# Optimization experiments

Measured on AMD Instinct MI355X. Metric: run time of the kernel, lower is better.

## Reference

```python
import jax, jax.numpy as jnp
import numpy as np

EPS = 1e-9
LN_EPS = 1e-5

def _ln(t, g, b):
    m = t.mean(-1, keepdims=True)
    v = ((t - m) ** 2).mean(-1, keepdims=True)
    return (t - m) / jnp.sqrt(v + LN_EPS) * g + b

def _dwconv(t, w, b):
    # t: (B,S,H), w: (H,1,4) depthwise. torch pads 3 on both sides then slices [:S],
    # which equals causal left-pad of 3.
    y = jax.lax.conv_general_dilated(
        t.transpose(0, 2, 1), w, window_strides=(1,), padding=[(3, 0)],
        feature_group_count=w.shape[0], dimension_numbers=("NCH", "OIH", "NCH"))
    return y.transpose(0, 2, 1) + b

def _forward(x, Wq, Wk, Wv, Wo, Wg, We1, We2, Wd1, Wd2, Wa1, Wa2,
             conv_w, conv_b, qn_g, qn_b, kn_g, kn_b, mW1, mb1, mW2, mb2, chunk_size):
    B, S, D = x.shape
    H = Wk.shape[1]
    M = mW1.shape[0]
    q = x @ Wq; k = x @ Wk; v = x @ Wv
    eta = jax.nn.softplus((x @ We1) @ We2)
    delta = jax.nn.softplus((x @ Wd1) @ Wd2)
    alpha = jax.nn.sigmoid((x @ Wa1) @ Wa2)
    q = _ln(_dwconv(q, conv_w, conv_b), qn_g, qn_b)  # computed but unused downstream, as in source
    k = _ln(_dwconv(k, conv_w, conv_b), kn_g, kn_b)
    v = _dwconv(v, conv_w, conv_b)
    n = S // chunk_size
    chunk = lambda t: t.reshape(B, n, chunk_size, H).transpose(1, 0, 2, 3)  # (n,B,C,H)
    xs = (chunk(k), chunk(v), chunk(eta), chunk(delta), chunk(alpha))
    state0 = (jnp.broadcast_to(mW1, (B, M, H)), jnp.broadcast_to(mb1, (B, M)),
              jnp.broadcast_to(mW2, (B, H, M)), jnp.broadcast_to(mb2, (B, H)))

    def step(state, inp):
        W1, b1, W2, b2 = state
        kc, vc, ec, dc, ac = inp  # each (B,C,H)
        inter = jnp.einsum("bch,bmh->bcm", kc, W1) + b1[:, None, :]
        act = jax.nn.gelu(inter, approximate=False)
        out = jnp.einsum("bcm,bhm->bch", act, W2) + b2[:, None, :]
        err = out - vc
        en = jnp.sqrt(jnp.sum(err * err, axis=-1, keepdims=True))  # (B,C,1)
        grad = jnp.where(en > dc, dc * err / (en + EPS), err)
        aw = ac[:, -1, :].mean(-1)[:, None, None]
        ew = ec[:, -1, :].mean(-1)[:, None, None]
        us = grad.mean(1, keepdims=True)   # (B,1,H)
        am = act.mean(1, keepdims=True)    # (B,1,M)
        W1g = jnp.einsum("bom,boh->bmh", am, us)
        W2g = jnp.einsum("boh,bom->bhm", us, am)
        nW1 = aw * W1 - ew * W1g
        nW2 = aw * W2 - ew * W2g
        ab = ac[:, -1, :]; eb = ec[:, -1, :]
        b2u = grad.mean(1)
        b1u = jnp.einsum("bch,bhm->bcm", grad, nW2).mean(1)
        nb2 = ab * b2 - eb * b2u
        nb1 = ab.mean(-1, keepdims=True) * b1 - eb.mean(-1, keepdims=True) * b1u
        # torch updates state under no_grad -> detach
        new_state = jax.tree_util.tree_map(jax.lax.stop_gradient, (nW1, nb1, nW2, nb2))
        return new_state, out

    _, outs = jax.lax.scan(step, state0, xs)  # (n,B,C,H)
    combined = outs.transpose(1, 0, 2, 3).reshape(B, S, H)
    return (combined @ Wo) * jax.nn.sigmoid(x @ Wg)

def setup_inputs():
    key = jax.random.key(0)
    B, S, D, H, M, R = 4, 4096, 1024, 128, 256, 64
    ks = jax.random.split(key, 23)
    g = lambda i, shp, s: jax.random.normal(ks[i], shp, jnp.float32) * s
    return {
        "x": g(0, (B, S, D), 1.0),
        "Wq": g(1, (D, H), 0.02), "Wk": g(2, (D, H), 0.02), "Wv": g(3, (D, H), 0.02),
        "Wo": g(4, (H, D), 0.02), "Wg": g(5, (D, D), 0.02),
        "We1": g(6, (D, R), 0.02), "We2": g(7, (R, H), 0.02),
        "Wd1": g(8, (D, R), 0.02), "Wd2": g(9, (R, H), 0.02),
        "Wa1": g(10, (D, R), 0.02), "Wa2": g(11, (R, H), 0.02),
        "conv_w": g(12, (H, 1, 4), 0.2), "conv_b": g(13, (H,), 0.02),
        "qn_g": jnp.ones((H,), jnp.float32), "qn_b": jnp.zeros((H,), jnp.float32),
        "kn_g": jnp.ones((H,), jnp.float32), "kn_b": jnp.zeros((H,), jnp.float32),
        "mW1": g(14, (M, H), 0.05), "mb1": g(15, (M,), 0.02),
        "mW2": g(16, (H, M), 0.05), "mb2": g(17, (H,), 0.02),
        "chunk_size": 64,
    }

def reference(x, Wq, Wk, Wv, Wo, Wg, We1, We2, Wd1, Wd2, Wa1, Wa2,
              conv_w, conv_b, qn_g, qn_b, kn_g, kn_b, mW1, mb1, mW2, mb2, chunk_size):
    return _forward(x, Wq, Wk, Wv, Wo, Wg, We1, We2, Wd1, Wd2, Wa1, Wa2,
                    conv_w, conv_b, qn_g, qn_b, kn_g, kn_b, mW1, mb1, mW2, mb2, chunk_size)
```

## Files before the change

kernel.cpp:

```cpp
#include <hip/hip_runtime.h>
#include <math.h>

#define Bq 4
#define Sq 4096
#define Dq 1024
#define Hq 128
#define Mq 256
#define Rq 64
#define Cq 64
#define NCHUNK 64
#define BSq (Bq*Sq)

typedef __attribute__((ext_vector_type(8))) short short8;
typedef __attribute__((ext_vector_type(4))) float f32x4;
typedef __attribute__((ext_vector_type(2))) unsigned int uintx2;

#define U_WKVTH  ((size_t)0)
#define U_WKVTL  (U_WKVTH + (size_t)2*Hq*Dq)
#define U_WEDATH (U_WKVTL + (size_t)2*Hq*Dq)
#define U_WEDATL (U_WEDATH + (size_t)3*Rq*Dq)
#define U_WGTH   (U_WEDATL + (size_t)3*Rq*Dq)
#define U_WGTL   (U_WGTH + (size_t)Dq*Dq)
#define U_WE2TH  (U_WGTL + (size_t)Dq*Dq)
#define U_WE2TL  (U_WE2TH + (size_t)Hq*Rq)
#define U_WD2TH  (U_WE2TL + (size_t)Hq*Rq)
#define U_WD2TL  (U_WD2TH + (size_t)Hq*Rq)
#define U_WA2TH  (U_WD2TL + (size_t)Hq*Rq)
#define U_WA2TL  (U_WA2TH + (size_t)Hq*Rq)
#define U_WOTH   (U_WA2TL + (size_t)Hq*Rq)
#define U_WOTL   (U_WOTH + (size_t)Dq*Hq)
#define U_END    (U_WOTL + (size_t)Dq*Hq)

__device__ __forceinline__ float softplusf_(float x){
  return fmaxf(x,0.f) + log1pf(expf(-fabsf(x)));
}
__device__ __forceinline__ float sigmoidf_(float x){
  return 1.f/(1.f+__expf(-x));
}
__device__ __forceinline__ unsigned short bf16rn(float x){
  unsigned u = __float_as_uint(x);
  u += 0x7fffu + ((u>>16)&1u);
  return (unsigned short)(u>>16);
}
__device__ __forceinline__ float bf16tof(unsigned short s){
  return __uint_as_float(((unsigned)s)<<16);
}
__device__ __forceinline__ unsigned cvt_pk_bf16(float a, float b){
  unsigned r;
  asm("v_cvt_pk_bf16_f32 %0, %1, %2" : "=v"(r) : "v"(a), "v"(b));
  return r;
}
__device__ __forceinline__ float lo16f(unsigned p){ return __uint_as_float(p<<16); }
__device__ __forceinline__ float hi16f(unsigned p){ return __uint_as_float(p & 0xffff0000u); }
union pk8 { unsigned u[4]; short8 s; };

__device__ __forceinline__ float gelu_fast(float x){
  float z  = x*0.70710678118f;
  float az = fabsf(z);
  float t  = __builtin_amdgcn_rcpf(fmaf(0.3275911f, az, 1.f));
  float p  = fmaf(t, 1.061405429f, -1.453152027f);
  p = fmaf(t, p, 1.421413741f);
  p = fmaf(t, p, -0.284496736f);
  p = fmaf(t, p, 0.254829592f);
  p = p*t;
  float e  = __expf(-az*az);
  float er = copysignf(1.f - p*e, z);
  return 0.5f*x*(1.f + er);
}

template<int BN, int ACT>
__global__ __launch_bounds__(256) void gemm_bf3(
    const float* __restrict__ Af,
    const unsigned short* __restrict__ BhT, const unsigned short* __restrict__ BlT,
    float* __restrict__ C, const float* __restrict__ gate, int N, int K)
{
  constexpr int BM = 128;
  constexpr int PK = 40;
  constexpr int TN = BN/32;
  __shared__ __align__(16) unsigned short As[2][BM*PK];
  __shared__ __align__(16) unsigned short Bs[2][BN*PK];
  const int tid = threadIdx.x;
  const int bm = blockIdx.y*BM, bn = blockIdx.x*BN;
  const int wv = tid>>6, lane = tid&63;
  const int n16 = lane&15, q = lane>>4;
  const int wm = wv>>1, wn = wv&1;

  f32x4 acc[4][TN];
  #pragma unroll
  for (int i=0;i<4;i++){
    #pragma unroll
    for (int j=0;j<TN;j++){ f32x4 z={0.f,0.f,0.f,0.f}; acc[i][j]=z; }
  }
  for (int k0=0;k0<K;k0+=32){
    #pragma unroll
    for (int c0=0;c0<BM*8;c0+=256){
      int c = c0 + tid;
      int row = c>>3, kg = (c&7)*4;
      float4 v = *(const float4*)&Af[(size_t)(bm+row)*K + k0+kg];
      unsigned hp0 = cvt_pk_bf16(v.x, v.y), hp1 = cvt_pk_bf16(v.z, v.w);
      unsigned lp0 = cvt_pk_bf16(v.x-lo16f(hp0), v.y-hi16f(hp0));
      unsigned lp1 = cvt_pk_bf16(v.z-lo16f(hp1), v.w-hi16f(hp1));
      int off = row*PK+kg;
      uintx2 th = {hp0, hp1}, tl = {lp0, lp1};
      *(uintx2*)&As[0][off] = th;
      *(uintx2*)&As[1][off] = tl;
    }
    #pragma unroll
    for (int c0=0;c0<BN*4;c0+=256){
      int c = c0 + tid;
      int row = c>>2, kg = (c&3)*8;
      *(short8*)&Bs[0][row*PK+kg] = *(const short8*)&BhT[(size_t)(bn+row)*K + k0+kg];
      *(short8*)&Bs[1][row*PK+kg] = *(const short8*)&BlT[(size_t)(bn+row)*K + k0+kg];
    }
    __syncthreads();
    short8 a_h[4], a_l[4], b_h[TN], b_l[TN];
    #pragma unroll
    for (int i=0;i<4;i++){
      int r = wm*64 + i*16 + n16;
      a_h[i] = *(const short8*)&As[0][r*PK + q*8];
      a_l[i] = *(const short8*)&As[1][r*PK + q*8];
    }
    #pragma unroll
    for (int j=0;j<TN;j++){
      int r = wn*(BN/2) + j*16 + n16;
      b_h[j] = *(const short8*)&Bs[0][r*PK + q*8];
      b_l[j] = *(const short8*)&Bs[1][r*PK + q*8];
    }
    #pragma unroll
    for (int i=0;i<4;i++){
      #pragma unroll
      for (int j=0;j<TN;j++){
        acc[i][j] = __builtin_amdgcn_mfma_f32_16x16x32_bf16(a_h[i], b_h[j], acc[i][j], 0,0,0);
        acc[i][j] = __builtin_amdgcn_mfma_f32_16x16x32_bf16(a_l[i], b_h[j], acc[i][j], 0,0,0);
        acc[i][j] = __builtin_amdgcn_mfma_f32_16x16x32_bf16(a_h[i], b_l[j], acc[i][j], 0,0,0);
      }
    }
    __syncthreads();
  }
  #pragma unroll
  for (int i=0;i<4;i++){
    #pragma unroll
    for (int j=0;j<TN;j++){
      #pragma unroll
      for (int r=0;r<4;r++){
        int row = bm + wm*64 + i*16 + q*4 + r;
        int col = bn + wn*(BN/2) + j*16 + n16;
        float v = acc[i][j][r];
        if (ACT==1) v = softplusf_(v);
        else if (ACT==2) v = sigmoidf_(v);
        else if (ACT==3) v *= sigmoidf_(gate[(size_t)row*N+col]);
        C[(size_t)row*N+col] = v;
      }
    }
  }
}

template<int BN>
__global__ __launch_bounds__(256) void gemm_bb(
    const unsigned short* __restrict__ Ah, const unsigned short* __restrict__ Al,
    const unsigned short* __restrict__ BhT, const unsigned short* __restrict__ BlT,
    float* __restrict__ C0, float* __restrict__ C1, float* __restrict__ C2, int K)
{
  constexpr int BM = 128;
  constexpr int PK = 40;
  constexpr int TN = BN/32;
  __shared__ __align__(16) unsigned short As[2][BM*PK];
  __shared__ __align__(16) unsigned short Bs[2][BN*PK];
  const int tid = threadIdx.x;
  const int bx = blockIdx.x;
  const int bm = blockIdx.y*BM;
  const int bnB = bx*BN;
  float* __restrict__ C = (bx==0) ? C0 : ((bx==1) ? C1 : C2);
  const int wv = tid>>6, lane = tid&63;
  const int n16 = lane&15, q = lane>>4;
  const int wm = wv>>1, wn = wv&1;

  f32x4 acc[4][TN];
  #pragma unroll
  for (int i=0;i<4;i++){
    #pragma unroll
    for (int j=0;j<TN;j++){ f32x4 z={0.f,0.f,0.f,0.f}; acc[i][j]=z; }
  }
  for (int k0=0;k0<K;k0+=32){
    #pragma unroll
    for (int c0=0;c0<BM*4;c0+=256){
      int c = c0 + tid;
      int row = c>>2, kg = (c&3)*8;
      *(short8*)&As[0][row*PK+kg] = *(const short8*)&Ah[(size_t)(bm+row)*K + k0+kg];
      *(short8*)&As[1][row*PK+kg] = *(const short8*)&Al[(size_t)(bm+row)*K + k0+kg];
    }
    #pragma unroll
    for (int c0=0;c0<BN*4;c0+=256){
      int c = c0 + tid;
      int row = c>>2, kg = (c&3)*8;
      *(short8*)&Bs[0][row*PK+kg] = *(const short8*)&BhT[(size_t)(bnB+row)*K + k0+kg];
      *(short8*)&Bs[1][row*PK+kg] = *(const short8*)&BlT[(size_t)(bnB+row)*K + k0+kg];
    }
    __syncthreads();
    short8 a_h[4], a_l[4], b_h[TN], b_l[TN];
    #pragma unroll
    for (int i=0;i<4;i++){
      int r = wm*64 + i*16 + n16;
      a_h[i] = *(const short8*)&As[0][r*PK + q*8];
      a_l[i] = *(const short8*)&As[1][r*PK + q*8];
    }
    #pragma unroll
    for (int j=0;j<TN;j++){
      int r = wn*(BN/2) + j*16 + n16;
      b_h[j] = *(const short8*)&Bs[0][r*PK + q*8];
      b_l[j] = *(const short8*)&Bs[1][r*PK + q*8];
    }
    #pragma unroll
    for (int i=0;i<4;i++){
      #pragma unroll
      for (int j=0;j<TN;j++){
        acc[i][j] = __builtin_amdgcn_mfma_f32_16x16x32_bf16(a_h[i], b_h[j], acc[i][j], 0,0,0);
        acc[i][j] = __builtin_amdgcn_mfma_f32_16x16x32_bf16(a_l[i], b_h[j], acc[i][j], 0,0,0);
        acc[i][j] = __builtin_amdgcn_mfma_f32_16x16x32_bf16(a_h[i], b_l[j], acc[i][j], 0,0,0);
      }
    }
    __syncthreads();
  }
  #pragma unroll
  for (int i=0;i<4;i++){
    #pragma unroll
    for (int j=0;j<TN;j++){
      #pragma unroll
      for (int r=0;r<4;r++){
        int row = bm + wm*64 + i*16 + q*4 + r;
        int col = wn*(BN/2) + j*16 + n16;
        C[(size_t)row*BN+col] = acc[i][j][r];
      }
    }
  }
}

__global__ __launch_bounds__(256) void gemm_eda2(
    const float* __restrict__ te, const float* __restrict__ td, const float* __restrict__ ta,
    const unsigned short* __restrict__ usb,
    float* __restrict__ etab, float* __restrict__ deltab, float* __restrict__ alphab)
{
  constexpr int BM = 128, PK = 40, BN = 128, TN = 4, K = Rq, N = Hq;
  __shared__ __align__(16) unsigned short As[2][BM*PK];
  __shared__ __align__(16) unsigned short Bs[2][BN*PK];
  const int tid = threadIdx.x;
  const int bx = blockIdx.x;
  const int bm = blockIdx.y*BM;
  const float* __restrict__ Af = (bx==0) ? te : (bx==1) ? td : ta;
  const unsigned short* __restrict__ BhT = usb + ((bx==0) ? U_WE2TH : (bx==1) ? U_WD2TH : U_WA2TH);
  const unsigned short* __restrict__ BlT = usb + ((bx==0) ? U_WE2TL : (bx==1) ? U_WD2TL : U_WA2TL);
  float* __restrict__ C = (bx==0) ? etab : (bx==1) ? deltab : alphab;
  const int wv = tid>>6, lane = tid&63;
  const int n16 = lane&15, q = lane>>4;
  const int wm = wv>>1, wn = wv&1;

  f32x4 acc[4][TN];
  #pragma unroll
  for (int i=0;i<4;i++){
    #pragma unroll
    for (int j=0;j<TN;j++){ f32x4 z={0.f,0.f,0.f,0.f}; acc[i][j]=z; }
  }
  for (int k0=0;k0<K;k0+=32){
    #pragma unroll
    for (int c0=0;c0<BM*8;c0+=256){
      int c = c0 + tid;
      int row = c>>3, kg = (c&7)*4;
      float4 v = *(const float4*)&Af[(size_t)(bm+row)*K + k0+kg];
      unsigned hp0 = cvt_pk_bf16(v.x, v.y), hp1 = cvt_pk_bf16(v.z, v.w);
      unsigned lp0 = cvt_pk_bf16(v.x-lo16f(hp0), v.y-hi16f(hp0));
      unsigned lp1 = cvt_pk_bf16(v.z-lo16f(hp1), v.w-hi16f(hp1));
      int off = row*PK+kg;
      uintx2 th = {hp0, hp1}, tl = {lp0, lp1};
      *(uintx2*)&As[0][off] = th;
      *(uintx2*)&As[1][off] = tl;
    }
    #pragma unroll
    for (int c0=0;c0<BN*4;c0+=256){
      int c = c0 + tid;
      int row = c>>2, kg = (c&3)*8;
      *(short8*)&Bs[0][row*PK+kg] = *(const short8*)&BhT[(size_t)row*K + k0+kg];
      *(short8*)&Bs[1][row*PK+kg] = *(const short8*)&BlT[(size_t)row*K + k0+kg];
    }
    __syncthreads();
    short8 a_h[4], a_l[4], b_h[TN], b_l[TN];
    #pragma unroll
    for (int i=0;i<4;i++){
      int r = wm*64 + i*16 + n16;
      a_h[i] = *(const short8*)&As[0][r*PK + q*8];
      a_l[i] = *(const short8*)&As[1][r*PK + q*8];
    }
    #pragma unroll
    for (int j=0;j<TN;j++){
      int r = wn*(BN/2) + j*16 + n16;
      b_h[j] = *(const short8*)&Bs[0][r*PK + q*8];
      b_l[j] = *(const short8*)&Bs[1][r*PK + q*8];
    }
    #pragma unroll
    for (int i=0;i<4;i++){
      #pragma unroll
      for (int j=0;j<TN;j++){
        acc[i][j] = __builtin_amdgcn_mfma_f32_16x16x32_bf16(a_h[i], b_h[j], acc[i][j], 0,0,0);
        acc[i][j] = __builtin_amdgcn_mfma_f32_16x16x32_bf16(a_l[i], b_h[j], acc[i][j], 0,0,0);
        acc[i][j] = __builtin_amdgcn_mfma_f32_16x16x32_bf16(a_h[i], b_l[j], acc[i][j], 0,0,0);
      }
    }
    __syncthreads();
  }
  #pragma unroll
  for (int i=0;i<4;i++){
    #pragma unroll
    for (int j=0;j<TN;j++){
      #pragma unroll
      for (int r=0;r<4;r++){
        int row = bm + wm*64 + i*16 + q*4 + r;
        int col = wn*(BN/2) + j*16 + n16;
        float v = acc[i][j][r];
        v = (bx==2) ? sigmoidf_(v) : softplusf_(v);
        C[(size_t)row*N+col] = v;
      }
    }
  }
}

__global__ __launch_bounds__(256) void splitT_all(
    const float* __restrict__ Wk,  const float* __restrict__ Wv,
    const float* __restrict__ We1, const float* __restrict__ Wd1,
    const float* __restrict__ Wa1, const float* __restrict__ Wg,
    const float* __restrict__ We2, const float* __restrict__ Wd2,
    const float* __restrict__ Wa2, const float* __restrict__ Wo,
    unsigned short* __restrict__ usb)
{
  size_t idx = (size_t)blockIdx.x*256 + threadIdx.x;
#define SEG(SRC, DH, DL, K_, N_) \
  { size_t sz = (size_t)(K_)*(N_); \
    if (idx < sz){ \
      int nn = (int)(idx/(K_)); int k = (int)(idx - (size_t)nn*(K_)); \
      float v = (SRC)[(size_t)k*(N_) + nn]; \
      unsigned short hh = bf16rn(v); \
      (DH)[idx] = hh; (DL)[idx] = bf16rn(v - bf16tof(hh)); \
      return; } \
    idx -= sz; }
  SEG(Wk,  usb+U_WKVTH,                    usb+U_WKVTL,                    Dq, Hq)
  SEG(Wv,  usb+U_WKVTH+(size_t)Hq*Dq,      usb+U_WKVTL+(size_t)Hq*Dq,      Dq, Hq)
  SEG(We1, usb+U_WEDATH,                   usb+U_WEDATL,                   Dq, Rq)
  SEG(Wd1, usb+U_WEDATH+(size_t)Rq*Dq,     usb+U_WEDATL+(size_t)Rq*Dq,     Dq, Rq)
  SEG(Wa1, usb+U_WEDATH+(size_t)2*Rq*Dq,   usb+U_WEDATL+(size_t)2*Rq*Dq,   Dq, Rq)
  SEG(Wg,  usb+U_WGTH,                     usb+U_WGTL,                     Dq, Dq)
  SEG(We2, usb+U_WE2TH,                    usb+U_WE2TL,                    Rq, Hq)
  SEG(Wd2, usb+U_WD2TH,                    usb+U_WD2TL,                    Rq, Hq)
  SEG(Wa2, usb+U_WA2TH,                    usb+U_WA2TL,                    Rq, Hq)
  SEG(Wo,  usb+U_WOTH,                     usb+U_WOTL,                     Hq, Dq)
#undef SEG
}

__global__ __launch_bounds__(256) void splitX(const float* __restrict__ A,
    unsigned short* __restrict__ h, unsigned short* __restrict__ l)
{
  size_t idx = ((size_t)blockIdx.x*256 + threadIdx.x)*4;
  float4 v = *(const float4*)&A[idx];
  unsigned hp0 = cvt_pk_bf16(v.x, v.y), hp1 = cvt_pk_bf16(v.z, v.w);
  unsigned lp0 = cvt_pk_bf16(v.x-lo16f(hp0), v.y-hi16f(hp0));
  unsigned lp1 = cvt_pk_bf16(v.z-lo16f(hp1), v.w-hi16f(hp1));
  uintx2 th = {hp0, hp1}, tl = {lp0, lp1};
  *(uintx2*)&h[idx] = th;
  *(uintx2*)&l[idx] = tl;
}

__global__ __launch_bounds__(128) void conv_ln_kernel(
  const float* __restrict__ k_raw, const float* __restrict__ v_raw,
  const float* __restrict__ conv_w, const float* __restrict__ conv_b,
  const float* __restrict__ kn_g, const float* __restrict__ kn_b,
  float* __restrict__ k_out, float* __restrict__ v_out)
{
  int s = blockIdx.x, b = blockIdx.y, which = blockIdx.z;
  int h = threadIdx.x;
  const float* src = (which==0) ? k_raw : v_raw;
  float acc = conv_b[h];
  #pragma unroll
  for (int j=0;j<4;j++){
    int ss = s-3+j;
    if (ss>=0) acc += conv_w[h*4+j]*src[((size_t)b*Sq+ss)*Hq + h];
  }
  if (which==0){
    __shared__ float red[4];
    float sv = acc, s2 = acc*acc;
    #pragma unroll
    for (int off=32; off>0; off>>=1){
      sv += __shfl_down(sv, off, 64);
      s2 += __shfl_down(s2, off, 64);
    }
    if ((h&63)==0){ red[(h>>6)*2]=sv; red[(h>>6)*2+1]=s2; }
    __syncthreads();
    float mean = (red[0]+red[2])*(1.f/128.f);
    float var  = (red[1]+red[3])*(1.f/128.f) - mean*mean;
    float y = (acc-mean)*rsqrtf(var+1e-5f)*kn_g[h]+kn_b[h];
    k_out[((size_t)b*Sq+s)*Hq + h] = y;
  } else {
    v_out[((size_t)b*Sq+s)*Hq + h] = acc;
  }
}

#define OFF_KCH   0
#define OFF_KCL   16384
#define OFF_ACTH  32768
#define OFF_SAM   65536
#define OFF_SUS   66560
#define OFF_PEN   67072
#define OFF_DRED  70144
#define OFF_SUU   78336
#define OFF_SAB   78368
#define OFF_SEB   78880
#define OFF_SABP  79392
#define OFF_SEBP  79400
#define LDS_TOTAL 79408

__global__ __launch_bounds__(512, 2) void fused_scan_wg(
  const float* __restrict__ k_ln, const float* __restrict__ v_c,
  const float* __restrict__ eta, const float* __restrict__ delta,
  const float* __restrict__ alpha,
  const float* __restrict__ mW1, const float* __restrict__ mb1,
  const float* __restrict__ mW2, const float* __restrict__ mb2,
  float* __restrict__ combined,
  const float* __restrict__ x,
  const unsigned short* __restrict__ WgTh, const unsigned short* __restrict__ WgTl,
  float* __restrict__ glog)
{
  __shared__ __align__(16) char smem[LDS_TOTAL];
  const int blk = blockIdx.x;
  const int tid = threadIdx.x;
  const int wv = tid >> 6;
  const int lane = tid & 63;
  const int n = lane & 15;
  const int q = lane >> 4;

  if (blk >= 4){
    unsigned short* As_h = (unsigned short*)smem;
    unsigned short* As_l = As_h + 128*40;
    unsigned short* Bs_h = As_l + 128*40;
    unsigned short* Bs_l = Bs_h + 128*40;
    const int g = blk - 4;
    const int bm = (g>>3)*128, bn = (g&7)*128;
    const int wm = wv&3, wn = wv>>2;
    f32x4 acc[2][4];
    #pragma unroll
    for (int i=0;i<2;i++){
      #pragma unroll
      for (int j=0;j<4;j++){ f32x4 z={0.f,0.f,0.f,0.f}; acc[i][j]=z; }
    }
    for (int k0=0;k0<Dq;k0+=32){
      #pragma unroll
      for (int r=0;r<2;r++){
        int idx = tid + 512*r;
        int row = idx>>3, kg = (idx&7)*4;
        float4 v = *(const float4*)&x[(size_t)(bm+row)*Dq + k0+kg];
        unsigned hp0 = cvt_pk_bf16(v.x, v.y), hp1 = cvt_pk_bf16(v.z, v.w);
        unsigned lp0 = cvt_pk_bf16(v.x-lo16f(hp0), v.y-hi16f(hp0));
        unsigned lp1 = cvt_pk_bf16(v.z-lo16f(hp1), v.w-hi16f(hp1));
        int off = row*40+kg;
        uintx2 th = {hp0, hp1}, tl = {lp0, lp1};
        *(uintx2*)&As_h[off] = th;
        *(uintx2*)&As_l[off] = tl;
      }
      {
        int row = tid>>2, kg = (tid&3)*8;
        *(short8*)&Bs_h[row*40+kg] = *(const short8*)&WgTh[(size_t)(bn+row)*Dq + k0+kg];
        *(short8*)&Bs_l[row*40+kg] = *(const short8*)&WgTl[(size_t)(bn+row)*Dq + k0+kg];
      }
      __syncthreads();
      short8 a_h[2], a_l[2], b_h[4], b_l[4];
      #pragma unroll
      for (int i=0;i<2;i++){
        int r = wm*32 + i*16 + n;
        a_h[i] = *(const short8*)&As_h[r*40 + q*8];
        a_l[i] = *(const short8*)&As_l[r*40 + q*8];
      }
      #pragma unroll
      for (int j=0;j<4;j++){
        int r = wn*64 + j*16 + n;
        b_h[j] = *(const short8*)&Bs_h[r*40 + q*8];
        b_l[j] = *(const short8*)&Bs_l[r*40 + q*8];
      }
      #pragma unroll
      for (int i=0;i<2;i++){
        #pragma unroll
        for (int j=0;j<4;j++){
          acc[i][j] = __builtin_amdgcn_mfma_f32_16x16x32_bf16(a_h[i], b_h[j], acc[i][j], 0,0,0);
          acc[i][j] = __builtin_amdgcn_mfma_f32_16x16x32_bf16(a_l[i], b_h[j], acc[i][j], 0,0,0);
          acc[i][j] = __builtin_amdgcn_mfma_f32_16x16x32_bf16(a_h[i], b_l[j], acc[i][j], 0,0,0);
        }
      }
      __syncthreads();
    }
    #pragma unroll
    for (int i=0;i<2;i++){
      #pragma unroll
      for (int j=0;j<4;j++){
        #pragma unroll
        for (int r=0;r<4;r++){
          int row = bm + wm*32 + i*16 + q*4 + r;
          int col = bn + wn*64 + j*16 + n;
          glog[(size_t)row*Dq+col] = acc[i][j][r];
        }
      }
    }
    return;
  }

  unsigned short* kc_hi  = (unsigned short*)(smem + OFF_KCH);
  unsigned short* kc_lo  = (unsigned short*)(smem + OFF_KCL);
  unsigned short* act_hi = (unsigned short*)(smem + OFF_ACTH);
  float* Sam = (float*)(smem + OFF_SAM);
  float* Sus = (float*)(smem + OFF_SUS);
  float* pen = (float*)(smem + OFF_PEN);
  float* Dred= (float*)(smem + OFF_DRED);
  float* Suu = (float*)(smem + OFF_SUU);
  float* Sab = (float*)(smem + OFF_SAB);
  float* Seb = (float*)(smem + OFF_SEB);
  float* Sabp = (float*)(smem + OFF_SABP);
  float* Sebp = (float*)(smem + OFF_SEBP);

  const int b = blk;
  const int h = wv*16 + n;
  float w1m[2][4][8];
  float w2m[8][8];
  float b1reg[2];
  float b2n[4];
  #pragma unroll
  for (int tt=0;tt<2;tt++){
    int m = (2*wv+tt)*16 + n;
    #pragma unroll
    for (int ks=0;ks<4;ks++){
      const float* p = mW1 + (size_t)m*Hq + ks*32 + q*8;
      #pragma unroll
      for (int j=0;j<8;j++) w1m[tt][ks][j] = p[j];
    }
    b1reg[tt] = mb1[m];
  }
  {
    #pragma unroll
    for (int ks2=0;ks2<8;ks2++){
      const float* p = mW2 + (size_t)h*Mq + ks2*32 + q*8;
      #pragma unroll
      for (int j=0;j<8;j++) w2m[ks2][j] = p[j];
    }
    #pragma unroll
    for (int r=0;r<4;r++) b2n[r] = mb2[wv*16 + q*4 + r];
  }
  float aw = 0.f, ew = 0.f;
  float am_own[2] = {0.f, 0.f};

  float4 pf[4];
  {
    const size_t base0 = (size_t)b*Sq*Hq;
    #pragma unroll
    for (int r4=0;r4<4;r4++){
      int i4 = tid + 512*r4;
      pf[r4] = *(const float4*)(k_ln + base0 + (size_t)i4*4);
    }
  }

  for (int t=0; t<NCHUNK; ++t){
    const size_t base = ((size_t)b*Sq + (size_t)t*Cq)*Hq;
    f32x4 vvv[4], ddd[4];
    #pragma unroll
    for (int ct=0;ct<4;ct++){
      size_t off = base + (size_t)(ct*16+n)*Hq + wv*16 + q*4;
      vvv[ct] = *(const f32x4*)&v_c[off];
      ddd[ct] = *(const f32x4*)&delta[off];
    }
    #pragma unroll
    for (int r4=0;r4<4;r4++){
      int i4 = tid + 512*r4;
      int c = i4>>5, h0 = (i4&31)<<2;
      float4 v = pf[r4];
      int pg  = (h0>>3) ^ (c & 15);
      int off = c*Hq + (pg<<3) + (h0&7);
      unsigned hp0 = cvt_pk_bf16(v.x, v.y), hp1 = cvt_pk_bf16(v.z, v.w);
      unsigned lp0 = cvt_pk_bf16(v.x-lo16f(hp0), v.y-hi16f(hp0));
      unsigned lp1 = cvt_pk_bf16(v.z-lo16f(hp1), v.w-hi16f(hp1));
      uintx2 th = {hp0, hp1}, tl = {lp0, lp1};
      *(uintx2*)&kc_hi[off] = th;
      *(uintx2*)&kc_lo[off] = tl;
    }
    float ab_=0.f, eb_=0.f;
    if (tid < 128){
      ab_ = alpha[base + 63*Hq + tid];
      eb_ = eta[base + 63*Hq + tid];
    }
    __syncthreads();

    if (t > 0){
      float4 s0[4], s1[4];
      #pragma unroll
      for (int ks=0;ks<4;ks++){
        s0[ks] = *(const float4*)&Sus[ks*32 + q*8];
        s1[ks] = *(const float4*)&Sus[ks*32 + q*8 + 4];
      }
      float4 u0 = *(const float4*)&Suu[0];
      float4 u1 = *(const float4*)&Suu[4];
      float uu = u0.x+u0.y+u0.z+u0.w+u1.x+u1.y+u1.z+u1.w;
      #pragma unroll
      for (int tt=0;tt<2;tt++){
        int m = (2*wv+tt)*16 + n;
        float amm = am_own[tt];
        float eam = ew*amm;
        #pragma unroll
        for (int ks=0;ks<4;ks++){
          #pragma unroll
          for (int j=0;j<4;j++){
            w1m[tt][ks][j]   = aw*w1m[tt][ks][j]   - eam*s0[ks][j];
            w1m[tt][ks][j+4] = aw*w1m[tt][ks][j+4] - eam*s1[ks][j];
          }
        }
        float dsum = 0.f;
        #pragma unroll
        for (int w8=0;w8<8;w8++) dsum += Dred[w8*256 + m];
        b1reg[tt] = aw*b1reg[tt] - ew*(aw*dsum - ew*uu*amm);
      }
    }

    f32x4 acc1[2][4];
    #pragma unroll
    for (int tt=0;tt<2;tt++){
      #pragma unroll
      for (int ct=0;ct<4;ct++){ f32x4 z={0.f,0.f,0.f,0.f}; acc1[tt][ct]=z; }
    }
    __builtin_amdgcn_s_setprio(1);
    #pragma unroll
    for (int ks=0;ks<4;ks++){
      pk8 BH[2], BL[2];
      #pragma unroll
      for (int tt=0;tt<2;tt++){
        #pragma unroll
        for (int jp=0;jp<4;jp++){
          float a0 = w1m[tt][ks][2*jp], a1 = w1m[tt][ks][2*jp+1];
          unsigned hp = cvt_pk_bf16(a0, a1);
          BH[tt].u[jp] = hp;
          BL[tt].u[jp] = cvt_pk_bf16(a0 - lo16f(hp), a1 - hi16f(hp));
        }
      }
      #pragma unroll
      for (int ct=0;ct<4;ct++){
        int c = ct*16 + n;
        int off = c*Hq + ((((ks*4+q)^n))<<3);
        short8 ah = *(const short8*)&kc_hi[off];
        short8 al = *(const short8*)&kc_lo[off];
        #pragma unroll
        for (int tt=0;tt<2;tt++){
          acc1[tt][ct] = __builtin_amdgcn_mfma_f32_16x16x32_bf16(ah, BH[tt].s, acc1[tt][ct], 0,0,0);
          acc1[tt][ct] = __builtin_amdgcn_mfma_f32_16x16x32_bf16(al, BH[tt].s, acc1[tt][ct], 0,0,0);
          acc1[tt][ct] = __builtin_amdgcn_mfma_f32_16x16x32_bf16(ah, BL[tt].s, acc1[tt][ct], 0,0,0);
        }
      }
    }
    __builtin_amdgcn_s_setprio(0);
    #pragma unroll
    for (int tt=0;tt<2;tt++){
      int m = (2*wv+tt)*16 + n;
      float b1v = b1reg[tt];
      float amsum = 0.f;
      #pragma unroll
      for (int ct=0;ct<4;ct++){
        #pragma unroll
        for (int r=0;r<4;r++){
          float g = gelu_fast(acc1[tt][ct][r] + b1v);
          amsum += g;
          int c = ct*16 + q*4 + r;
          int pg = (m>>3) ^ (c & 15);
          act_hi[c*Mq + (pg<<3) + (m&7)] = bf16rn(g);
        }
      }
      amsum += __shfl_xor(amsum, 16, 64);
      amsum += __shfl_xor(amsum, 32, 64);
      am_own[tt] = amsum*(1.f/64.f);
      if (q==0) Sam[m] = am_own[tt];
    }
    if (tid < 128){ Sab[tid] = ab_; Seb[tid] = eb_; }
    if (wv < 2){
      float a2 = ab_, e2 = eb_;
      #pragma unroll
      for (int mk=1;mk<64;mk<<=1){ a2 += __shfl_xor(a2,mk,64); e2 += __shfl_xor(e2,mk,64); }
      if (lane==0){ Sabp[wv] = a2; Sebp[wv] = e2; }
    }
    __syncthreads();

    f32x4 acc2[4];
    #pragma unroll
    for (int ct=0;ct<4;ct++){ f32x4 z={0.f,0.f,0.f,0.f}; acc2[ct]=z; }
    __builtin_amdgcn_s_setprio(1);
    #pragma unroll
    for (int ks2=0;ks2<8;ks2++){
      pk8 BH, BL;
      #pragma unroll
      for (int jp=0;jp<4;jp++){
        float a0 = w2m[ks2][2*jp], a1 = w2m[ks2][2*jp+1];
        unsigned hp = cvt_pk_bf16(a0, a1);
        BH.u[jp] = hp;
        BL.u[jp] = cvt_pk_bf16(a0 - lo16f(hp), a1 - hi16f(hp));
      }
      #pragma unroll
      for (int ct=0;ct<4;ct++){
        int c = ct*16 + n;
        int off = c*Mq + ((((ks2*4+q)^n))<<3);
        short8 ah = *(const short8*)&act_hi[off];
        acc2[ct] = __builtin_amdgcn_mfma_f32_16x16x32_bf16(BH.s, ah, acc2[ct], 0,0,0);
        acc2[ct] = __builtin_amdgcn_mfma_f32_16x16x32_bf16(BL.s, ah, acc2[ct], 0,0,0);
      }
    }
    __builtin_amdgcn_s_setprio(0);

    {
      const size_t basen = ((size_t)b*Sq + (size_t)((t+1<NCHUNK)?(t+1):t)*Cq)*Hq;
      #pragma unroll
      for (int r4=0;r4<4;r4++){
        int i4 = tid + 512*r4;
        pf[r4] = *(const float4*)(k_ln + basen + (size_t)i4*4);
      }
    }

    float err[4][4];
    {
      float* cb = combined + base;
      #pragma unroll
      for (int ct=0;ct<4;ct++){
        int c = ct*16 + n;
        f32x4 ov;
        #pragma unroll
        for (int r=0;r<4;r++){
          float o = acc2[ct][r] + b2n[r];
          ov[r] = o;
          err[ct][r] = o - vvv[ct][r];
        }
        *(f32x4*)&cb[(size_t)c*Hq + wv*16 + q*4] = ov;
      }
      #pragma unroll
      for (int ct=0;ct<4;ct++){
        float s = err[ct][0]*err[ct][0] + err[ct][1]*err[ct][1]
                + err[ct][2]*err[ct][2] + err[ct][3]*err[ct][3];
        s += __shfl_xor(s, 16, 64);
        s += __shfl_xor(s, 32, 64);
        if (q==0) pen[(ct*16+n)*12 + wv] = s;
      }
    }
    __syncthreads();

    aw = (Sabp[0]+Sabp[1])*(1.f/128.f);
    ew = (Sebp[0]+Sebp[1])*(1.f/128.f);

    float en_c[4];
    #pragma unroll
    for (int ct=0;ct<4;ct++){
      int c = ct*16 + n;
      float4 e0 = *(const float4*)&pen[c*12];
      float4 e1 = *(const float4*)&pen[c*12+4];
      en_c[ct] = sqrtf(e0.x+e0.y+e0.z+e0.w+e1.x+e1.y+e1.z+e1.w);
    }
    float us_r[4];
    #pragma unroll
    for (int r=0;r<4;r++){
      float s = 0.f;
      #pragma unroll
      for (int ct=0;ct<4;ct++){
        float e = err[ct][r];
        float dvv = ddd[ct][r];
        float en = en_c[ct];
        float g = (en > dvv) ? dvv*e*__builtin_amdgcn_rcpf(en+1e-9f) : e;
        s += g;
      }
      s += __shfl_xor(s,1,64); s += __shfl_xor(s,2,64);
      s += __shfl_xor(s,4,64); s += __shfl_xor(s,8,64);
      us_r[r] = s*(1.f/64.f);
    }
    if (n==0){
      #pragma unroll
      for (int r=0;r<4;r++) Sus[wv*16 + q*4 + r] = us_r[r];
    }
    {
      float uun = us_r[0]*us_r[0] + us_r[1]*us_r[1]
                + us_r[2]*us_r[2] + us_r[3]*us_r[3];
      uun += __shfl_xor(uun, 16, 64);
      uun += __shfl_xor(uun, 32, 64);
      if (lane==0) Suu[wv] = uun;
    }
    {
      f32x4 sab = *(const f32x4*)&Sab[wv*16 + q*4];
      f32x4 seb = *(const f32x4*)&Seb[wv*16 + q*4];
      #pragma unroll
      for (int r=0;r<4;r++) b2n[r] = sab[r]*b2n[r] - seb[r]*us_r[r];
    }
    float ush;
    {
      int src = (n>>2)<<4;
      float p0 = __shfl(us_r[0], src, 64);
      float p1 = __shfl(us_r[1], src, 64);
      float p2 = __shfl(us_r[2], src, 64);
      float p3 = __shfl(us_r[3], src, 64);
      int rr = n&3;
      ush = (rr==0) ? p0 : (rr==1) ? p1 : (rr==2) ? p2 : p3;
    }

    {
      const bool bb0 = (n&1);
      float p1[8][4];
      #pragma unroll
      for (int k2=0;k2<8;k2++){
        #pragma unroll
        for (int l=0;l<4;l++){
          float mine = ush * (bb0 ? w2m[k2][l+4] : w2m[k2][l]);
          float oth  = ush * (bb0 ? w2m[k2][l]   : w2m[k2][l+4]);
          p1[k2][l] = mine + __shfl_xor(oth, 1, 64);
        }
      }
      const bool bb1 = (n>>1)&1;
      float p2[4][4];
      #pragma unroll
      for (int k2=0;k2<4;k2++){
        #pragma unroll
        for (int l=0;l<4;l++){
          float mine = bb1 ? p1[2*k2+1][l] : p1[2*k2][l];
          float oth  = bb1 ? p1[2*k2][l]   : p1[2*k2+1][l];
          p2[k2][l] = mine + __shfl_xor(oth, 2, 64);
        }
      }
      const bool bb2 = (n>>2)&1;
      float p3[2][4];
      #pragma unroll
      for (int k2=0;k2<2;k2++){
        #pragma unroll
        for (int l=0;l<4;l++){
          float mine = bb2 ? p2[2*k2+1][l] : p2[2*k2][l];
          float oth  = bb2 ? p2[2*k2][l]   : p2[2*k2+1][l];
          p3[k2][l] = mine + __shfl_xor(oth, 4, 64);
        }
      }
      const bool bb3 = (n>>3)&1;
      float4 p4;
      {
        float m0 = bb3 ? p3[1][0] : p3[0][0];
        float o0 = bb3 ? p3[0][0] : p3[1][0];
        p4.x = m0 + __shfl_xor(o0, 8, 64);
        float m1 = bb3 ? p3[1][1] : p3[0][1];
        float o1 = bb3 ? p3[0][1] : p3[1][1];
        p4.y = m1 + __shfl_xor(o1, 8, 64);
        float m2 = bb3 ? p3[1][2] : p3[0][2];
        float o2 = bb3 ? p3[0][2] : p3[1][2];
        p4.z = m2 + __shfl_xor(o2, 8, 64);
        float m3 = bb3 ? p3[1][3] : p3[0][3];
        float o3 = bb3 ? p3[0][3] : p3[1][3];
        p4.w = m3 + __shfl_xor(o3, 8, 64);
      }
      int base_m = (n>>1)*32 + q*8 + (n&1)*4;
      *(float4*)&Dred[wv*256 + base_m] = p4;
    }

    {
      float eus = ew*ush;
      #pragma unroll
      for (int ks2=0;ks2<8;ks2++){
        float4 a0 = *(const float4*)&Sam[ks2*32 + q*8];
        float4 a1 = *(const float4*)&Sam[ks2*32 + q*8 + 4];
        #pragma unroll
        for (int j=0;j<4;j++){
          w2m[ks2][j]   = aw*w2m[ks2][j]   - eus*a0[j];
          w2m[ks2][j+4] = aw*w2m[ks2][j+4] - eus*a1[j];
        }
      }
    }
  }
}

extern "C" void kernel_launch(void* const* d_in, const int* in_sizes, int n_in,
                              void* d_out, int out_size, void* d_ws, size_t ws_size,
                              hipStream_t stream)
{
  const float* x    = (const float*)d_in[0];
  const float* Wk   = (const float*)d_in[2];
  const float* Wv   = (const float*)d_in[3];
  const float* Wo   = (const float*)d_in[4];
  const float* Wg   = (const float*)d_in[5];
  const float* We1  = (const float*)d_in[6];
  const float* We2  = (const float*)d_in[7];
  const float* Wd1  = (const float*)d_in[8];
  const float* Wd2  = (const float*)d_in[9];
  const float* Wa1  = (const float*)d_in[10];
  const float* Wa2  = (const float*)d_in[11];
  const float* conv_w = (const float*)d_in[12];
  const float* conv_b = (const float*)d_in[13];
  const float* kn_g = (const float*)d_in[16];
  const float* kn_b = (const float*)d_in[17];
  const float* mW1  = (const float*)d_in[18];
  const float* mb1  = (const float*)d_in[19];
  const float* mW2  = (const float*)d_in[20];
  const float* mb2  = (const float*)d_in[21];
  float* out = (float*)d_out;

  float* ws = (float*)d_ws;
  size_t o = 0;
  float* k_raw = ws + o; o += (size_t)BSq*Hq;
  float* v_raw = ws + o; o += (size_t)BSq*Hq;
  float* te    = ws + o; o += (size_t)BSq*Rq;
  float* td    = ws + o; o += (size_t)BSq*Rq;
  float* ta    = ws + o; o += (size_t)BSq*Rq;
  float* glog  = ws + o; o += (size_t)BSq*Dq;
  float* etab  = ws + o; o += (size_t)BSq*Hq;
  float* deltab= ws + o; o += (size_t)BSq*Hq;
  float* alphab= ws + o; o += (size_t)BSq*Hq;
  float* k_ln  = ws + o; o += (size_t)BSq*Hq;
  float* v_c   = ws + o; o += (size_t)BSq*Hq;
  float* comb  = ws + o; o += (size_t)BSq*Hq;
  unsigned short* usb = (unsigned short*)(ws + o);

  unsigned short* xh = (unsigned short*)glog;
  unsigned short* xl = xh + (size_t)BSq*Dq;

  {
    size_t total = 2*(size_t)Hq*Dq + 3*(size_t)Rq*Dq + (size_t)Dq*Dq
                 + 3*(size_t)Hq*Rq + (size_t)Dq*Hq;
    splitT_all<<<(unsigned)(total/256), 256, 0, stream>>>(
        Wk, Wv, We1, Wd1, Wa1, Wg, We2, Wd2, Wa2, Wo, usb);
  }
  splitX<<<(size_t)BSq*Dq/4/256, 256, 0, stream>>>(x, xh, xl);

  dim3 blk(256);
  gemm_bb<128><<<dim3(2, BSq/128), blk, 0, stream>>>(xh, xl, usb+U_WKVTH, usb+U_WKVTL, k_raw, v_raw, nullptr, Dq);
  gemm_bb<64> <<<dim3(3, BSq/128), blk, 0, stream>>>(xh, xl, usb+U_WEDATH, usb+U_WEDATL, te, td, ta, Dq);
  gemm_eda2<<<dim3(3, BSq/128), blk, 0, stream>>>(te, td, ta, usb, etab, deltab, alphab);
  conv_ln_kernel<<<dim3(Sq, Bq, 2), dim3(128), 0, stream>>>(
      k_raw, v_raw, conv_w, conv_b, kn_g, kn_b, k_ln, v_c);
  fused_scan_wg<<<dim3(4 + (BSq/128)*(Dq/128)), dim3(512), 0, stream>>>(
      k_ln, v_c, etab, deltab, alphab, mW1, mb1, mW2, mb2, comb,
      x, usb+U_WGTH, usb+U_WGTL, glog);
  gemm_bf3<128,3><<<dim3(Dq/128, BSq/128), blk, 0, stream>>>(comb, usb+U_WOTH, usb+U_WOTL, out, glog, Dq, Hq);
}
```

Before: 1.307 ms.

## Precompute bf16 hi/lo k in conv_ln, read directly in scan, recompute b1 update via transposed W2

```diff
diff --git a/kernel.cpp b/kernel.cpp
--- a/kernel.cpp
+++ b/kernel.cpp
@@ -370,7 +370,8 @@
   const float* __restrict__ k_raw, const float* __restrict__ v_raw,
   const float* __restrict__ conv_w, const float* __restrict__ conv_b,
   const float* __restrict__ kn_g, const float* __restrict__ kn_b,
-  float* __restrict__ k_out, float* __restrict__ v_out)
+  unsigned short* __restrict__ khi, unsigned short* __restrict__ klo,
+  float* __restrict__ v_out)
 {
   int s = blockIdx.x, b = blockIdx.y, which = blockIdx.z;
   int h = threadIdx.x;
@@ -394,28 +395,28 @@
     float mean = (red[0]+red[2])*(1.f/128.f);
     float var  = (red[1]+red[3])*(1.f/128.f) - mean*mean;
     float y = (acc-mean)*rsqrtf(var+1e-5f)*kn_g[h]+kn_b[h];
-    k_out[((size_t)b*Sq+s)*Hq + h] = y;
+    unsigned short hh = bf16rn(y);
+    size_t idx = ((size_t)b*Sq+s)*Hq + h;
+    khi[idx] = hh;
+    klo[idx] = bf16rn(y - bf16tof(hh));
   } else {
     v_out[((size_t)b*Sq+s)*Hq + h] = acc;
   }
 }
 
-#define OFF_KCH   0
-#define OFF_KCL   16384
-#define OFF_ACTH  32768
-#define OFF_SAM   65536
-#define OFF_SUS   66560
-#define OFF_PEN   67072
-#define OFF_DRED  70144
-#define OFF_SUU   78336
-#define OFF_SAB   78368
-#define OFF_SEB   78880
-#define OFF_SABP  79392
-#define OFF_SEBP  79400
-#define LDS_TOTAL 79408
-
-__global__ __launch_bounds__(512, 2) void fused_scan_wg(
-  const float* __restrict__ k_ln, const float* __restrict__ v_c,
+#define OFF_ACTH  0
+#define OFF_SAM   32768
+#define OFF_SUS   33792
+#define OFF_PEN   34304
+#define OFF_SAB   37376
+#define OFF_SEB   37888
+#define OFF_SABP  38400
+#define OFF_SEBP  38408
+#define LDS_TOTAL 40960
+
+__global__ __launch_bounds__(512, 1) void fused_scan_wg(
+  const unsigned short* __restrict__ khi, const unsigned short* __restrict__ klo,
+  const float* __restrict__ v_c,
   const float* __restrict__ eta, const float* __restrict__ delta,
   const float* __restrict__ alpha,
   const float* __restrict__ mW1, const float* __restrict__ mb1,
@@ -506,14 +507,10 @@
     return;
   }
 
-  unsigned short* kc_hi  = (unsigned short*)(smem + OFF_KCH);
-  unsigned short* kc_lo  = (unsigned short*)(smem + OFF_KCL);
   unsigned short* act_hi = (unsigned short*)(smem + OFF_ACTH);
   float* Sam = (float*)(smem + OFF_SAM);
   float* Sus = (float*)(smem + OFF_SUS);
   float* pen = (float*)(smem + OFF_PEN);
-  float* Dred= (float*)(smem + OFF_DRED);
-  float* Suu = (float*)(smem + OFF_SUU);
   float* Sab = (float*)(smem + OFF_SAB);
   float* Seb = (float*)(smem + OFF_SEB);
   float* Sabp = (float*)(smem + OFF_SABP);
@@ -523,6 +520,7 @@
   const int h = wv*16 + n;
   float w1m[2][4][8];
   float w2m[8][8];
+  float w2t[2][4][8];
   float b1reg[2];
   float b2n[4];
   #pragma unroll
@@ -533,6 +531,8 @@
       const float* p = mW1 + (size_t)m*Hq + ks*32 + q*8;
       #pragma unroll
       for (int j=0;j<8;j++) w1m[tt][ks][j] = p[j];
+      #pragma unroll
+      for (int j=0;j<8;j++) w2t[tt][ks][j] = mW2[(size_t)(ks*32+q*8+j)*Mq + m];
     }
     b1reg[tt] = mb1[m];
   }
@@ -549,45 +549,19 @@
   float aw = 0.f, ew = 0.f;
   float am_own[2] = {0.f, 0.f};
 
-  float4 pf[4];
-  {
-    const size_t base0 = (size_t)b*Sq*Hq;
-    #pragma unroll
-    for (int r4=0;r4<4;r4++){
-      int i4 = tid + 512*r4;
-      pf[r4] = *(const float4*)(k_ln + base0 + (size_t)i4*4);
-    }
-  }
+  const unsigned short* khb = khi + (size_t)b*Sq*Hq;
+  const unsigned short* klb = klo + (size_t)b*Sq*Hq;
 
   for (int t=0; t<NCHUNK; ++t){
     const size_t base = ((size_t)b*Sq + (size_t)t*Cq)*Hq;
-    f32x4 vvv[4], ddd[4];
-    #pragma unroll
-    for (int ct=0;ct<4;ct++){
-      size_t off = base + (size_t)(ct*16+n)*Hq + wv*16 + q*4;
-      vvv[ct] = *(const f32x4*)&v_c[off];
-      ddd[ct] = *(const f32x4*)&delta[off];
-    }
-    #pragma unroll
-    for (int r4=0;r4<4;r4++){
-      int i4 = tid + 512*r4;
-      int c = i4>>5, h0 = (i4&31)<<2;
-      float4 v = pf[r4];
-      int pg  = (h0>>3) ^ (c & 15);
-      int off = c*Hq + (pg<<3) + (h0&7);
-      unsigned hp0 = cvt_pk_bf16(v.x, v.y), hp1 = cvt_pk_bf16(v.z, v.w);
-      unsigned lp0 = cvt_pk_bf16(v.x-lo16f(hp0), v.y-hi16f(hp0));
-      unsigned lp1 = cvt_pk_bf16(v.z-lo16f(hp1), v.w-hi16f(hp1));
-      uintx2 th = {hp0, hp1}, tl = {lp0, lp1};
-      *(uintx2*)&kc_hi[off] = th;
-      *(uintx2*)&kc_lo[off] = tl;
-    }
+    const size_t kcb  = (size_t)t*Cq*Hq;
+    __syncthreads();
+
     float ab_=0.f, eb_=0.f;
     if (tid < 128){
       ab_ = alpha[base + 63*Hq + tid];
       eb_ = eta[base + 63*Hq + tid];
     }
-    __syncthreads();
 
     if (t > 0){
       float4 s0[4], s1[4];
@@ -596,26 +570,27 @@
         s0[ks] = *(const float4*)&Sus[ks*32 + q*8];
         s1[ks] = *(const float4*)&Sus[ks*32 + q*8 + 4];
       }
-      float4 u0 = *(const float4*)&Suu[0];
-      float4 u1 = *(const float4*)&Suu[4];
-      float uu = u0.x+u0.y+u0.z+u0.w+u1.x+u1.y+u1.z+u1.w;
       #pragma unroll
       for (int tt=0;tt<2;tt++){
-        int m = (2*wv+tt)*16 + n;
         float amm = am_own[tt];
         float eam = ew*amm;
+        float part = 0.f;
         #pragma unroll
         for (int ks=0;ks<4;ks++){
           #pragma unroll
           for (int j=0;j<4;j++){
-            w1m[tt][ks][j]   = aw*w1m[tt][ks][j]   - eam*s0[ks][j];
-            w1m[tt][ks][j+4] = aw*w1m[tt][ks][j+4] - eam*s1[ks][j];
+            float su0 = s0[ks][j], su1 = s1[ks][j];
+            w1m[tt][ks][j]   = aw*w1m[tt][ks][j]   - eam*su0;
+            w1m[tt][ks][j+4] = aw*w1m[tt][ks][j+4] - eam*su1;
+            float nw0 = aw*w2t[tt][ks][j]   - ew*su0*amm;
+            float nw1 = aw*w2t[tt][ks][j+4] - ew*su1*amm;
+            w2t[tt][ks][j] = nw0;  w2t[tt][ks][j+4] = nw1;
+            part += su0*nw0 + su1*nw1;
           }
         }
-        float dsum = 0.f;
-        #pragma unroll
-        for (int w8=0;w8<8;w8++) dsum += Dred[w8*256 + m];
-        b1reg[tt] = aw*b1reg[tt] - ew*(aw*dsum - ew*uu*amm);
+        part += __shfl_xor(part, 16, 64);
+        part += __shfl_xor(part, 32, 64);
+        b1reg[tt] = aw*b1reg[tt] - ew*part;
       }
     }
 
@@ -641,10 +616,9 @@
       }
       #pragma unroll
       for (int ct=0;ct<4;ct++){
-        int c = ct*16 + n;
-        int off = c*Hq + ((((ks*4+q)^n))<<3);
-        short8 ah = *(const short8*)&kc_hi[off];
-        short8 al = *(const short8*)&kc_lo[off];
+        size_t off = kcb + (size_t)(ct*16+n)*Hq + (ks*4+q)*8;
+        short8 ah = *(const short8*)&khb[off];
+        short8 al = *(const short8*)&klb[off];
         #pragma unroll
         for (int tt=0;tt<2;tt++){
           acc1[tt][ct] = __builtin_amdgcn_mfma_f32_16x16x32_bf16(ah, BH[tt].s, acc1[tt][ct], 0,0,0);
@@ -684,6 +658,22 @@
     }
     __syncthreads();
 
+    f32x4 vvv[4], ddd[4];
+    #pragma unroll
+    for (int ct=0;ct<4;ct++){
+      size_t off = base + (size_t)(ct*16+n)*Hq + wv*16 + q*4;
+      vvv[ct] = *(const f32x4*)&v_c[off];
+      ddd[ct] = *(const f32x4*)&delta[off];
+    }
+    {
+      size_t nb = (size_t)((t+1<NCHUNK)?(t+1):t)*Cq*Hq;
+      short8 t0 = *(const short8*)&khb[nb + tid*8];
+      short8 t1 = *(const short8*)&khb[nb + 4096 + tid*8];
+      short8 t2 = *(const short8*)&klb[nb + tid*8];
+      short8 t3 = *(const short8*)&klb[nb + 4096 + tid*8];
+      asm volatile("" :: "v"((int)t0[0]), "v"((int)t1[0]), "v"((int)t2[0]), "v"((int)t3[0]));
+    }
+
     f32x4 acc2[4];
     #pragma unroll
     for (int ct=0;ct<4;ct++){ f32x4 z={0.f,0.f,0.f,0.f}; acc2[ct]=z; }
@@ -708,15 +698,6 @@
       }
     }
     __builtin_amdgcn_s_setprio(0);
-
-    {
-      const size_t basen = ((size_t)b*Sq + (size_t)((t+1<NCHUNK)?(t+1):t)*Cq)*Hq;
-      #pragma unroll
-      for (int r4=0;r4<4;r4++){
-        int i4 = tid + 512*r4;
-        pf[r4] = *(const float4*)(k_ln + basen + (size_t)i4*4);
-      }
-    }
 
     float err[4][4];
     {
@@ -776,13 +757,6 @@
       for (int r=0;r<4;r++) Sus[wv*16 + q*4 + r] = us_r[r];
     }
     {
-      float uun = us_r[0]*us_r[0] + us_r[1]*us_r[1]
-                + us_r[2]*us_r[2] + us_r[3]*us_r[3];
-      uun += __shfl_xor(uun, 16, 64);
-      uun += __shfl_xor(uun, 32, 64);
-      if (lane==0) Suu[wv] = uun;
-    }
-    {
       f32x4 sab = *(const f32x4*)&Sab[wv*16 + q*4];
       f32x4 seb = *(const f32x4*)&Seb[wv*16 + q*4];
       #pragma unroll
@@ -798,61 +772,6 @@
       int rr = n&3;
       ush = (rr==0) ? p0 : (rr==1) ? p1 : (rr==2) ? p2 : p3;
     }
-
-    {
-      const bool bb0 = (n&1);
-      float p1[8][4];
-      #pragma unroll
-      for (int k2=0;k2<8;k2++){
-        #pragma unroll
-        for (int l=0;l<4;l++){
-          float mine = ush * (bb0 ? w2m[k2][l+4] : w2m[k2][l]);
-          float oth  = ush * (bb0 ? w2m[k2][l]   : w2m[k2][l+4]);
-          p1[k2][l] = mine + __shfl_xor(oth, 1, 64);
-        }
-      }
-      const bool bb1 = (n>>1)&1;
-      float p2[4][4];
-      #pragma unroll
-      for (int k2=0;k2<4;k2++){
-        #pragma unroll
-        for (int l=0;l<4;l++){
-          float mine = bb1 ? p1[2*k2+1][l] : p1[2*k2][l];
-          float oth  = bb1 ? p1[2*k2][l]   : p1[2*k2+1][l];
-          p2[k2][l] = mine + __shfl_xor(oth, 2, 64);
-        }
-      }
-      const bool bb2 = (n>>2)&1;
-      float p3[2][4];
-      #pragma unroll
-      for (int k2=0;k2<2;k2++){
-        #pragma unroll
-        for (int l=0;l<4;l++){
-          float mine = bb2 ? p2[2*k2+1][l] : p2[2*k2][l];
-          float oth  = bb2 ? p2[2*k2][l]   : p2[2*k2+1][l];
-          p3[k2][l] = mine + __shfl_xor(oth, 4, 64);
-        }
-      }
-      const bool bb3 = (n>>3)&1;
-      float4 p4;
-      {
-        float m0 = bb3 ? p3[1][0] : p3[0][0];
-        float o0 = bb3 ? p3[0][0] : p3[1][0];
-        p4.x = m0 + __shfl_xor(o0, 8, 64);
-        float m1 = bb3 ? p3[1][1] : p3[0][1];
-        float o1 = bb3 ? p3[0][1] : p3[1][1];
-        p4.y = m1 + __shfl_xor(o1, 8, 64);
-        float m2 = bb3 ? p3[1][2] : p3[0][2];
-        float o2 = bb3 ? p3[0][2] : p3[1][2];
-        p4.z = m2 + __shfl_xor(o2, 8, 64);
-        float m3 = bb3 ? p3[1][3] : p3[0][3];
-        float o3 = bb3 ? p3[0][3] : p3[1][3];
-        p4.w = m3 + __shfl_xor(o3, 8, 64);
-      }
-      int base_m = (n>>1)*32 + q*8 + (n&1)*4;
-      *(float4*)&Dred[wv*256 + base_m] = p4;
-    }
-
     {
       float eus = ew*ush;
       #pragma unroll
@@ -905,10 +824,13 @@
   float* etab  = ws + o; o += (size_t)BSq*Hq;
   float* deltab= ws + o; o += (size_t)BSq*Hq;
   float* alphab= ws + o; o += (size_t)BSq*Hq;
-  float* k_ln  = ws + o; o += (size_t)BSq*Hq;
+  float* kslot = ws + o; o += (size_t)BSq*Hq;
   float* v_c   = ws + o; o += (size_t)BSq*Hq;
   float* comb  = ws + o; o += (size_t)BSq*Hq;
   unsigned short* usb = (unsigned short*)(ws + o);
+
+  unsigned short* khi = (unsigned short*)kslot;
+  unsigned short* klo = khi + (size_t)BSq*Hq;
 
   unsigned short* xh = (unsigned short*)glog;
   unsigned short* xl = xh + (size_t)BSq*Dq;
@@ -926,9 +848,9 @@
   gemm_bb<64> <<<dim3(3, BSq/128), blk, 0, stream>>>(xh, xl, usb+U_WEDATH, usb+U_WEDATL, te, td, ta, Dq);
   gemm_eda2<<<dim3(3, BSq/128), blk, 0, stream>>>(te, td, ta, usb, etab, deltab, alphab);
   conv_ln_kernel<<<dim3(Sq, Bq, 2), dim3(128), 0, stream>>>(
-      k_raw, v_raw, conv_w, conv_b, kn_g, kn_b, k_ln, v_c);
+      k_raw, v_raw, conv_w, conv_b, kn_g, kn_b, khi, klo, v_c);
   fused_scan_wg<<<dim3(4 + (BSq/128)*(Dq/128)), dim3(512), 0, stream>>>(
-      k_ln, v_c, etab, deltab, alphab, mW1, mb1, mW2, mb2, comb,
+      khi, klo, v_c, etab, deltab, alphab, mW1, mb1, mW2, mb2, comb,
       x, usb+U_WGTH, usb+U_WGTL, glog);
   gemm_bf3<128,3><<<dim3(Dq/128, BSq/128), blk, 0, stream>>>(comb, usb+U_WOTH, usb+U_WOTL, out, glog, Dq, Hq);
 }
```

After: 2.009 ms. 53.7% more time.

## Pre-split k into bf16 hi/lo in conv_ln and stream via global_load_lds

Applied to the files above, without the earlier changes.

```diff
diff --git a/kernel.cpp b/kernel.cpp
--- a/kernel.cpp
+++ b/kernel.cpp
@@ -53,6 +53,13 @@
 __device__ __forceinline__ float lo16f(unsigned p){ return __uint_as_float(p<<16); }
 __device__ __forceinline__ float hi16f(unsigned p){ return __uint_as_float(p & 0xffff0000u); }
 union pk8 { unsigned u[4]; short8 s; };
+
+__device__ __forceinline__ void g2lds16(const unsigned short* g, void* lds){
+  __builtin_amdgcn_global_load_lds(
+      (const __attribute__((address_space(1))) unsigned int*)(const void*)g,
+      (__attribute__((address_space(3))) unsigned int*)lds,
+      16, 0, 0);
+}
 
 __device__ __forceinline__ float gelu_fast(float x){
   float z  = x*0.70710678118f;
@@ -370,7 +377,8 @@
   const float* __restrict__ k_raw, const float* __restrict__ v_raw,
   const float* __restrict__ conv_w, const float* __restrict__ conv_b,
   const float* __restrict__ kn_g, const float* __restrict__ kn_b,
-  float* __restrict__ k_out, float* __restrict__ v_out)
+  unsigned short* __restrict__ khi, unsigned short* __restrict__ klo,
+  float* __restrict__ v_out)
 {
   int s = blockIdx.x, b = blockIdx.y, which = blockIdx.z;
   int h = threadIdx.x;
@@ -394,7 +402,10 @@
     float mean = (red[0]+red[2])*(1.f/128.f);
     float var  = (red[1]+red[3])*(1.f/128.f) - mean*mean;
     float y = (acc-mean)*rsqrtf(var+1e-5f)*kn_g[h]+kn_b[h];
-    k_out[((size_t)b*Sq+s)*Hq + h] = y;
+    unsigned short hh = bf16rn(y);
+    size_t idx = ((size_t)b*Sq+s)*Hq + h;
+    khi[idx] = hh;
+    klo[idx] = bf16rn(y - bf16tof(hh));
   } else {
     v_out[((size_t)b*Sq+s)*Hq + h] = acc;
   }
@@ -415,7 +426,8 @@
 #define LDS_TOTAL 79408
 
 __global__ __launch_bounds__(512, 2) void fused_scan_wg(
-  const float* __restrict__ k_ln, const float* __restrict__ v_c,
+  const unsigned short* __restrict__ khi, const unsigned short* __restrict__ klo,
+  const float* __restrict__ v_c,
   const float* __restrict__ eta, const float* __restrict__ delta,
   const float* __restrict__ alpha,
   const float* __restrict__ mW1, const float* __restrict__ mb1,
@@ -549,15 +561,21 @@
   float aw = 0.f, ew = 0.f;
   float am_own[2] = {0.f, 0.f};
 
-  float4 pf[4];
-  {
-    const size_t base0 = (size_t)b*Sq*Hq;
-    #pragma unroll
-    for (int r4=0;r4<4;r4++){
-      int i4 = tid + 512*r4;
-      pf[r4] = *(const float4*)(k_ln + base0 + (size_t)i4*4);
-    }
-  }
+  const unsigned short* khb = khi + (size_t)b*Sq*Hq;
+  const unsigned short* klb = klo + (size_t)b*Sq*Hq;
+
+  const int c0s = (wv*2+0)*4 + (lane>>4);
+  const int c1s = (wv*2+1)*4 + (lane>>4);
+  const int soff0 = c0s*Hq + ((((lane&15)^(c0s&15)))<<3);
+  const int soff1 = c1s*Hq + ((((lane&15)^(c1s&15)))<<3);
+  char* d_kh0 = smem + OFF_KCH + (wv*2+0)*1024;
+  char* d_kh1 = smem + OFF_KCH + (wv*2+1)*1024;
+  char* d_kl0 = smem + OFF_KCL + (wv*2+0)*1024;
+  char* d_kl1 = smem + OFF_KCL + (wv*2+1)*1024;
+  g2lds16(khb + soff0, d_kh0);
+  g2lds16(khb + soff1, d_kh1);
+  g2lds16(klb + soff0, d_kl0);
+  g2lds16(klb + soff1, d_kl1);
 
   for (int t=0; t<NCHUNK; ++t){
     const size_t base = ((size_t)b*Sq + (size_t)t*Cq)*Hq;
@@ -567,20 +585,6 @@
       size_t off = base + (size_t)(ct*16+n)*Hq + wv*16 + q*4;
       vvv[ct] = *(const f32x4*)&v_c[off];
       ddd[ct] = *(const f32x4*)&delta[off];
-    }
-    #pragma unroll
-    for (int r4=0;r4<4;r4++){
-      int i4 = tid + 512*r4;
-      int c = i4>>5, h0 = (i4&31)<<2;
-      float4 v = pf[r4];
-      int pg  = (h0>>3) ^ (c & 15);
-      int off = c*Hq + (pg<<3) + (h0&7);
-      unsigned hp0 = cvt_pk_bf16(v.x, v.y), hp1 = cvt_pk_bf16(v.z, v.w);
-      unsigned lp0 = cvt_pk_bf16(v.x-lo16f(hp0), v.y-hi16f(hp0));
-      unsigned lp1 = cvt_pk_bf16(v.z-lo16f(hp1), v.w-hi16f(hp1));
-      uintx2 th = {hp0, hp1}, tl = {lp0, lp1};
-      *(uintx2*)&kc_hi[off] = th;
-      *(uintx2*)&kc_lo[off] = tl;
     }
     float ab_=0.f, eb_=0.f;
     if (tid < 128){
@@ -684,6 +688,14 @@
     }
     __syncthreads();
 
+    {
+      const size_t nb = (size_t)((t+1<NCHUNK)?(t+1):t)*Cq*Hq;
+      g2lds16(khb + nb + soff0, d_kh0);
+      g2lds16(khb + nb + soff1, d_kh1);
+      g2lds16(klb + nb + soff0, d_kl0);
+      g2lds16(klb + nb + soff1, d_kl1);
+    }
+
     f32x4 acc2[4];
     #pragma unroll
     for (int ct=0;ct<4;ct++){ f32x4 z={0.f,0.f,0.f,0.f}; acc2[ct]=z; }
@@ -708,15 +720,6 @@
       }
     }
     __builtin_amdgcn_s_setprio(0);
-
-    {
-      const size_t basen = ((size_t)b*Sq + (size_t)((t+1<NCHUNK)?(t+1):t)*Cq)*Hq;
-      #pragma unroll
-      for (int r4=0;r4<4;r4++){
-        int i4 = tid + 512*r4;
-        pf[r4] = *(const float4*)(k_ln + basen + (size_t)i4*4);
-      }
-    }
 
     float err[4][4];
     {
@@ -905,10 +908,13 @@
   float* etab  = ws + o; o += (size_t)BSq*Hq;
   float* deltab= ws + o; o += (size_t)BSq*Hq;
   float* alphab= ws + o; o += (size_t)BSq*Hq;
-  float* k_ln  = ws + o; o += (size_t)BSq*Hq;
+  float* kslot = ws + o; o += (size_t)BSq*Hq;
   float* v_c   = ws + o; o += (size_t)BSq*Hq;
   float* comb  = ws + o; o += (size_t)BSq*Hq;
   unsigned short* usb = (unsigned short*)(ws + o);
+
+  unsigned short* khi = (unsigned short*)kslot;
+  unsigned short* klo = khi + (size_t)BSq*Hq;
 
   unsigned short* xh = (unsigned short*)glog;
   unsigned short* xl = xh + (size_t)BSq*Dq;
@@ -926,9 +932,9 @@
   gemm_bb<64> <<<dim3(3, BSq/128), blk, 0, stream>>>(xh, xl, usb+U_WEDATH, usb+U_WEDATL, te, td, ta, Dq);
   gemm_eda2<<<dim3(3, BSq/128), blk, 0, stream>>>(te, td, ta, usb, etab, deltab, alphab);
   conv_ln_kernel<<<dim3(Sq, Bq, 2), dim3(128), 0, stream>>>(
-      k_raw, v_raw, conv_w, conv_b, kn_g, kn_b, k_ln, v_c);
+      k_raw, v_raw, conv_w, conv_b, kn_g, kn_b, khi, klo, v_c);
   fused_scan_wg<<<dim3(4 + (BSq/128)*(Dq/128)), dim3(512), 0, stream>>>(
-      k_ln, v_c, etab, deltab, alphab, mW1, mb1, mW2, mb2, comb,
+      khi, klo, v_c, etab, deltab, alphab, mW1, mb1, mW2, mb2, comb,
       x, usb+U_WGTH, usb+U_WGTL, glog);
   gemm_bf3<128,3><<<dim3(Dq/128, BSq/128), blk, 0, stream>>>(comb, usb+U_WOTH, usb+U_WOTL, out, glog, Dq, Hq);
 }
```

New measurement: 1.371 ms. 1.05x slower.
